# Kernel tuning notes

Hardware: AMD Instinct MI355X
Metric: run time of the kernel (lower is better)

The kernel has to match this reference:

```python
import jax, jax.numpy as jnp
import numpy as np

B, S, D, H, FF = 4, 2048, 1024, 16, 4096
HD = D // H
EPS = 1e-5


def layer_norm(x, g, b):
    mu = jnp.mean(x, axis=-1, keepdims=True)
    var = jnp.mean(jnp.square(x - mu), axis=-1, keepdims=True)
    return (x - mu) * jax.lax.rsqrt(var + EPS) * g + b


def setup_inputs() -> dict:
    key = jax.random.key(0)
    ks = jax.random.split(key, 8)
    s_d = 1.0 / np.sqrt(D)
    s_ff = 1.0 / np.sqrt(FF)
    return {
        "x": jax.random.normal(ks[0], (B, S, D), dtype=jnp.float32),
        "Wq": jax.random.normal(ks[1], (D, D), dtype=jnp.float32) * s_d,
        "bq": jnp.zeros((D,), jnp.float32),
        "Wk": jax.random.normal(ks[2], (D, D), dtype=jnp.float32) * s_d,
        "bk": jnp.zeros((D,), jnp.float32),
        "Wv": jax.random.normal(ks[3], (D, D), dtype=jnp.float32) * s_d,
        "bv": jnp.zeros((D,), jnp.float32),
        "g1": jnp.ones((D,), jnp.float32),
        "beta1": jnp.zeros((D,), jnp.float32),
        "g2": jnp.ones((D,), jnp.float32),
        "beta2": jnp.zeros((D,), jnp.float32),
        "W1": jax.random.normal(ks[4], (D, FF), dtype=jnp.float32) * s_d,
        "b1": jnp.zeros((FF,), jnp.float32),
        "W2": jax.random.normal(ks[5], (FF, D), dtype=jnp.float32) * s_ff,
        "b2": jnp.zeros((D,), jnp.float32),
    }


def reference(x, Wq, bq, Wk, bk, Wv, bv, g1, beta1, g2, beta2, W1, b1, W2, b2):
    # pre-LN attention (self.layer_norm in the original)
    h = layer_norm(x, g1, beta1)
    q = (h @ Wq + bq).reshape(B, S, H, HD)
    k = (h @ Wk + bk).reshape(B, S, H, HD)
    v = (h @ Wv + bv).reshape(B, S, H, HD)
    scores = jnp.einsum("bqhd,bkhd->bhqk", q, k) / np.sqrt(HD)
    probs = jax.nn.softmax(scores, axis=-1)
    attn = jnp.einsum("bhqk,bkhd->bqhd", probs, v).reshape(B, S, D)
    y = attn + x
    # second LN (self.LN), then FFN; note original adds residual from LN output
    f = layer_norm(y, g2, beta2)
    ff = jnp.maximum(f @ W1 + b1, 0.0) @ W2 + b2
    return f + ff
```

## Files before the change

### kernel.cpp

```cpp
#include <hip/hip_runtime.h>
#include <hip/hip_bf16.h>
#include <cstdint>
#include <cstddef>

#define B_   4
#define S_   2048
#define D_   1024
#define H_   16
#define HD_  64
#define FF_  4096
#define MTOT (B_*S_)

typedef __bf16 bf16;
typedef bf16  bf16x8 __attribute__((ext_vector_type(8)));
typedef bf16  bf16x4 __attribute__((ext_vector_type(4)));
typedef float f32x4  __attribute__((ext_vector_type(4)));

#define LOG2E 1.44269504088896340736f

__device__ __forceinline__ void async16(const bf16* g, bf16* l) {
  __builtin_amdgcn_global_load_lds(
      (const __attribute__((address_space(1))) unsigned int*)g,
      (__attribute__((address_space(3))) unsigned int*)l,
      16, 0, 0);
}

__global__ void wcast_t(const float* __restrict__ W, bf16* __restrict__ Wt,
                        int K, int N) {
  __shared__ float t[32][33];
  const int k0 = blockIdx.y * 32, n0 = blockIdx.x * 32;
  const int tx = threadIdx.x, ty = threadIdx.y;
#pragma unroll
  for (int r = ty; r < 32; r += 8)
    t[r][tx] = W[(size_t)(k0 + r) * N + n0 + tx];
  __syncthreads();
#pragma unroll
  for (int r = ty; r < 32; r += 8)
    Wt[(size_t)(n0 + r) * K + k0 + tx] = (bf16)t[tx][r];
}

__global__ void ln_fused(const float* __restrict__ xin, const float* __restrict__ res,
                         const float* __restrict__ gamma, const float* __restrict__ beta,
                         bf16* __restrict__ out) {
  const int row = blockIdx.x, tid = threadIdx.x;
  const int lane = tid & 63, w = tid >> 6;
  f32x4 v = *(const f32x4*)(xin + (size_t)row * D_ + tid * 4);
  if (res) {
    f32x4 r = *(const f32x4*)(res + (size_t)row * D_ + tid * 4);
    v += r;
  }
  float sum = v[0] + v[1] + v[2] + v[3];
  float sq  = v[0]*v[0] + v[1]*v[1] + v[2]*v[2] + v[3]*v[3];
#pragma unroll
  for (int d = 1; d < 64; d <<= 1) {
    sum += __shfl_xor(sum, d);
    sq  += __shfl_xor(sq, d);
  }
  __shared__ float red[8];
  if (lane == 0) { red[w] = sum; red[4 + w] = sq; }
  __syncthreads();
  sum = red[0] + red[1] + red[2] + red[3];
  sq  = red[4] + red[5] + red[6] + red[7];
  const float mu   = sum * (1.f / D_);
  const float rstd = rsqrtf(sq * (1.f / D_) - mu * mu + 1e-5f);
  f32x4 g  = *(const f32x4*)(gamma + tid * 4);
  f32x4 bt = *(const f32x4*)(beta  + tid * 4);
  bf16x4 ov;
#pragma unroll
  for (int j = 0; j < 4; j++)
    ov[j] = (bf16)((v[j] - mu) * rstd * g[j] + bt[j]);
  *(bf16x4*)(out + (size_t)row * D_ + tid * 4) = ov;
}

template <int EPI>
__global__ __launch_bounds__(512)
void gemm256(const bf16* __restrict__ A, const bf16* __restrict__ Bt,
             const float* __restrict__ bias, void* __restrict__ Cout,
             const bf16* __restrict__ addf,
             const float* __restrict__ bq, const float* __restrict__ bk,
             const float* __restrict__ bv, bf16* __restrict__ qout,
             bf16* __restrict__ kout, bf16* __restrict__ vtout,
             int M, int N, int K) {
  __shared__ bf16 As[2][256 * 64];
  __shared__ bf16 Bs[2][256 * 64];
  const int tid = threadIdx.x;
  const int lane = tid & 63;
  const int w = tid >> 6;
  const int wm = w >> 2, wn = w & 3;
  const int rg = lane >> 4, rl = lane & 15;
  const int sr = lane >> 3;
  const int sc = (lane & 7) ^ sr;

  const int nbn = N >> 8;
  const int cpx = (int)gridDim.x >> 3;
  const int bid = (int)blockIdx.x;
  const int swz = (bid & 7) * cpx + (bid >> 3);
  const int bm = (swz / nbn) << 8;
  const int bn = (swz % nbn) << 8;

  const bf16* gA0 = A  + (size_t)(bm + w * 8 + sr) * K + sc * 8;
  const bf16* gB0 = Bt + (size_t)(bn + w * 8 + sr) * K + sc * 8;
  const size_t i64K = (size_t)64 * K;

#define GSTAGE(slot, t)                                                        \
  {                                                                            \
    const bf16* ga_ = gA0 + (size_t)(t) * 64;                                  \
    const bf16* gb_ = gB0 + (size_t)(t) * 64;                                  \
    _Pragma("unroll")                                                          \
    for (int i_ = 0; i_ < 4; i_++) {                                           \
      async16(ga_ + i_ * i64K, &As[slot][(i_ * 64 + w * 8) * 64]);             \
      async16(gb_ + i_ * i64K, &Bs[slot][(i_ * 64 + w * 8) * 64]);             \
    }                                                                          \
  }

#define COMPUTE(slotbuf)                                                       \
  {                                                                            \
    const bf16* Ac = &As[slotbuf][0];                                          \
    const bf16* Bc = &Bs[slotbuf][0];                                          \
    _Pragma("unroll")                                                          \
    for (int kk = 0; kk < 2; kk++) {                                           \
      bf16x8 af[8], bw[4];                                                     \
      _Pragma("unroll")                                                        \
      for (int mi = 0; mi < 8; mi++)                                           \
        af[mi] = *(const bf16x8*)(Ac + (wm * 128 + mi * 16 + rl) * 64 +        \
                                  (((kk * 4 + rg) ^ (rl & 7)) * 8));           \
      _Pragma("unroll")                                                        \
      for (int ni = 0; ni < 4; ni++)                                           \
        bw[ni] = *(const bf16x8*)(Bc + (wn * 64 + ni * 16 + rl) * 64 +         \
                                  (((kk * 4 + rg) ^ (rl & 7)) * 8));           \
      _Pragma("unroll")                                                        \
      for (int mi = 0; mi < 8; mi++)                                           \
        _Pragma("unroll")                                                      \
        for (int ni = 0; ni < 4; ni++)                                         \
          acc[mi][ni] = __builtin_amdgcn_mfma_f32_16x16x32_bf16(               \
              af[mi], bw[ni], acc[mi][ni], 0, 0, 0);                           \
    }                                                                          \
  }

  f32x4 acc[8][4];
  const f32x4 z = {0.f, 0.f, 0.f, 0.f};
#pragma unroll
  for (int mi = 0; mi < 8; mi++)
#pragma unroll
    for (int ni = 0; ni < 4; ni++) acc[mi][ni] = z;

  const int NT = K >> 6;
  GSTAGE(0, 0);
  GSTAGE(1, 1);

  for (int t = 0; t < NT - 1; ++t) {
    asm volatile("s_waitcnt vmcnt(8)" ::: "memory");
    __builtin_amdgcn_sched_barrier(0);
    __builtin_amdgcn_s_barrier();
    __builtin_amdgcn_sched_barrier(0);
    COMPUTE(t & 1);
    __builtin_amdgcn_sched_barrier(0);
    __builtin_amdgcn_s_barrier();
    __builtin_amdgcn_sched_barrier(0);
    if (t + 2 < NT) GSTAGE(t & 1, t + 2);
  }
  asm volatile("s_waitcnt vmcnt(0)" ::: "memory");
  __builtin_amdgcn_sched_barrier(0);
  __builtin_amdgcn_s_barrier();
  __builtin_amdgcn_sched_barrier(0);
  COMPUTE((NT - 1) & 1);

#undef GSTAGE
#undef COMPUTE

#pragma unroll
  for (int mi = 0; mi < 8; mi++) {
    const int row0 = bm + wm * 128 + mi * 16 + rg * 4;
#pragma unroll
    for (int ni = 0; ni < 4; ni++) {
      const int col = bn + wn * 64 + ni * 16 + rl;
      if (EPI == 3) {
        const float bb = bias[col];
#pragma unroll
        for (int i = 0; i < 4; i++)
          ((bf16*)Cout)[(size_t)(row0 + i) * N + col] =
              (bf16)fmaxf(acc[mi][ni][i] + bb, 0.f);
      } else if (EPI == 4) {
        const float bb = bias[col];
#pragma unroll
        for (int i = 0; i < 4; i++)
          ((float*)Cout)[(size_t)(row0 + i) * N + col] =
              acc[mi][ni][i] + bb + (float)addf[(size_t)(row0 + i) * N + col];
      } else {
        const int sector = bn >> 10;
        const int cl = col & 1023;
        const float bb = (sector == 0) ? bq[cl] : (sector == 1 ? bk[cl] : bv[cl]);
#pragma unroll
        for (int i = 0; i < 4; i++) {
          const int row = row0 + i;
          const float v = acc[mi][ni][i] + bb;
          if (sector == 0) {
            qout[(size_t)row * D_ + cl] = (bf16)(v * (0.125f * LOG2E));
          } else if (sector == 1) {
            kout[(size_t)row * D_ + cl] = (bf16)v;
          } else {
            const int b = row >> 11, s = row & 2047;
            const int h = cl >> 6, hd = cl & 63;
            vtout[(((size_t)(b * H_ + h) * HD_ + hd) << 11) + s] = (bf16)v;
          }
        }
      }
    }
  }
}

__global__ __launch_bounds__(512, 4)
void attn_fwd(const bf16* __restrict__ Q, const bf16* __restrict__ Kb,
              const bf16* __restrict__ Vt, float* __restrict__ O) {
  __shared__ bf16 Ks[2][64 * 64];
  __shared__ bf16 Vs[2][64 * 64];
  __shared__ bf16 Pl[8][32][72];
  const int tid = threadIdx.x, lane = tid & 63, w = tid >> 6;
  const int rg = lane >> 4, rl = lane & 15;
  const int bh = blockIdx.y, b = bh >> 4, h = bh & 15;
  const int q0 = blockIdx.x * 256 + w * 32;

  const bf16* qp = Q + ((size_t)b * S_ + q0) * D_ + h * HD_;
  const bf16* kp = Kb + (size_t)b * S_ * D_ + h * HD_;
  const bf16* vp = Vt + (size_t)bh * HD_ * S_;

  const int sr = lane >> 3;
  const int sc = (lane & 7) ^ sr;

#define STAGE(buf, t)                                                          \
  {                                                                            \
    const int row = w * 8 + sr;                                                \
    async16(kp + (size_t)((t) * 64 + row) * D_ + sc * 8, &Ks[buf][w * 8 * 64]);\
    async16(vp + (size_t)row * S_ + (t) * 64 + sc * 8,  &Vs[buf][w * 8 * 64]); \
  }

  bf16x8 qf[2][2];
#pragma unroll
  for (int m = 0; m < 2; m++)
#pragma unroll
    for (int kc = 0; kc < 2; kc++)
      qf[m][kc] = *(const bf16x8*)(qp + (size_t)(m * 16 + rl) * D_ + kc * 32 + rg * 8);

  const f32x4 z = {0.f, 0.f, 0.f, 0.f};
  f32x4 o[2][4];
  float mr[2], lr[2];
#pragma unroll
  for (int m = 0; m < 2; m++) {
    mr[m] = -1e30f; lr[m] = 0.f;
#pragma unroll
    for (int np = 0; np < 4; np++) o[m][np] = z;
  }

  STAGE(0, 0);
  __syncthreads();

  int cur = 0;
  for (int t = 0; t < S_ / 64; ++t) {
    if (t + 1 < S_ / 64) STAGE(cur ^ 1, t + 1);
    const bf16* Kc = Ks[cur];
    const bf16* Vc = Vs[cur];

    bf16x8 kf[4][2];
#pragma unroll
    for (int n = 0; n < 4; n++) {
      const int krow = n * 16 + rl;
#pragma unroll
      for (int kc = 0; kc < 2; kc++)
        kf[n][kc] = *(const bf16x8*)(Kc + krow * 64 + (((kc * 4 + rg) ^ (krow & 7)) * 8));
    }

    f32x4 s[2][4];
#pragma unroll
    for (int m = 0; m < 2; m++)
#pragma unroll
      for (int n = 0; n < 4; n++) s[m][n] = z;
#pragma unroll
    for (int kc = 0; kc < 2; kc++)
#pragma unroll
      for (int n = 0; n < 4; n++)
#pragma unroll
        for (int m = 0; m < 2; m++)
          s[m][n] = __builtin_amdgcn_mfma_f32_16x16x32_bf16(kf[n][kc], qf[m][kc], s[m][n], 0, 0, 0);

#pragma unroll
    for (int m = 0; m < 2; m++) {
      float x0 = fmaxf(fmaxf(s[m][0][0], s[m][0][1]), fmaxf(s[m][0][2], s[m][0][3]));
      float x1 = fmaxf(fmaxf(s[m][1][0], s[m][1][1]), fmaxf(s[m][1][2], s[m][1][3]));
      float x2 = fmaxf(fmaxf(s[m][2][0], s[m][2][1]), fmaxf(s[m][2][2], s[m][2][3]));
      float x3 = fmaxf(fmaxf(s[m][3][0], s[m][3][1]), fmaxf(s[m][3][2], s[m][3][3]));
      float vmax = fmaxf(fmaxf(x0, x1), fmaxf(x2, x3));
      vmax = fmaxf(vmax, __shfl_xor(vmax, 16));
      vmax = fmaxf(vmax, __shfl_xor(vmax, 32));
      const float mnew = fmaxf(mr[m], vmax);
      const float corr = __builtin_amdgcn_exp2f(mr[m] - mnew);
      mr[m] = mnew;
      float ps = 0.f;
#pragma unroll
      for (int n = 0; n < 4; n++)
#pragma unroll
        for (int i = 0; i < 4; i++) {
          const float p = __builtin_amdgcn_exp2f(s[m][n][i] - mnew);
          s[m][n][i] = p;
          ps += p;
        }
      ps += __shfl_xor(ps, 16);
      ps += __shfl_xor(ps, 32);
      lr[m] = lr[m] * corr + ps;
#pragma unroll
      for (int np = 0; np < 4; np++)
#pragma unroll
        for (int i = 0; i < 4; i++) o[m][np][i] *= corr;
#pragma unroll
      for (int n = 0; n < 4; n++) {
        bf16x4 pv;
#pragma unroll
        for (int i = 0; i < 4; i++) pv[i] = (bf16)s[m][n][i];
        *(bf16x4*)&Pl[w][m * 16 + rl][n * 16 + rg * 4] = pv;
      }
    }

    bf16x8 pf[2][2];
#pragma unroll
    for (int m = 0; m < 2; m++)
#pragma unroll
      for (int kc = 0; kc < 2; kc++)
        pf[m][kc] = *(const bf16x8*)&Pl[w][m * 16 + rl][kc * 32 + rg * 8];

    bf16x8 vf[4][2];
#pragma unroll
    for (int np = 0; np < 4; np++) {
      const int vrow = np * 16 + rl;
#pragma unroll
      for (int kc = 0; kc < 2; kc++)
        vf[np][kc] = *(const bf16x8*)(Vc + vrow * 64 + (((kc * 4 + rg) ^ (vrow & 7)) * 8));
    }

#pragma unroll
    for (int kc = 0; kc < 2; kc++)
#pragma unroll
      for (int np = 0; np < 4; np++)
#pragma unroll
        for (int m = 0; m < 2; m++)
          o[m][np] = __builtin_amdgcn_mfma_f32_16x16x32_bf16(vf[np][kc], pf[m][kc], o[m][np], 0, 0, 0);

    __syncthreads();
    cur ^= 1;
  }
#undef STAGE

#pragma unroll
  for (int m = 0; m < 2; m++) {
    const float inv = 1.f / lr[m];
    const size_t rowb = ((size_t)b * S_ + q0 + m * 16 + rl) * D_ + h * HD_;
#pragma unroll
    for (int np = 0; np < 4; np++) {
      f32x4 ov;
#pragma unroll
      for (int i = 0; i < 4; i++) ov[i] = o[m][np][i] * inv;
      *(f32x4*)(O + rowb + np * 16 + rg * 4) = ov;
    }
  }
}

extern "C" void kernel_launch(void* const* d_in, const int* in_sizes, int n_in,
                              void* d_out, int out_size, void* d_ws, size_t ws_size,
                              hipStream_t stream) {
  (void)in_sizes; (void)n_in; (void)out_size; (void)ws_size;
  const float* x   = (const float*)d_in[0];
  const float* Wq  = (const float*)d_in[1];
  const float* bq  = (const float*)d_in[2];
  const float* Wk  = (const float*)d_in[3];
  const float* bk  = (const float*)d_in[4];
  const float* Wv  = (const float*)d_in[5];
  const float* bv  = (const float*)d_in[6];
  const float* g1  = (const float*)d_in[7];
  const float* be1 = (const float*)d_in[8];
  const float* g2  = (const float*)d_in[9];
  const float* be2 = (const float*)d_in[10];
  const float* W1  = (const float*)d_in[11];
  const float* b1  = (const float*)d_in[12];
  const float* W2  = (const float*)d_in[13];
  const float* b2  = (const float*)d_in[14];
  float* out = (float*)d_out;

  char* p = (char*)d_ws;
  const size_t MB = (size_t)1 << 20;
  bf16*  wqkv = (bf16*)(p + 0 * MB);
  bf16*  w1t  = (bf16*)(p + 6 * MB);
  bf16*  w2t  = (bf16*)(p + 14 * MB);
  bf16*  hb   = (bf16*)(p + 22 * MB);
  bf16*  qb   = (bf16*)(p + 38 * MB);
  bf16*  kb   = (bf16*)(p + 54 * MB);
  bf16*  vt   = (bf16*)(p + 70 * MB);
  float* at   = (float*)(p + 86 * MB);
  bf16*  fb   = (bf16*)(p + 118 * MB);
  bf16*  ff1  = (bf16*)(p + 22 * MB);

  const dim3 tb(32, 8);
  wcast_t<<<dim3(32, 32),  tb, 0, stream>>>(Wq, wqkv,                1024, 1024);
  wcast_t<<<dim3(32, 32),  tb, 0, stream>>>(Wk, wqkv + 1024 * 1024,  1024, 1024);
  wcast_t<<<dim3(32, 32),  tb, 0, stream>>>(Wv, wqkv + 2048 * 1024,  1024, 1024);
  wcast_t<<<dim3(128, 32), tb, 0, stream>>>(W1, w1t, 1024, 4096);
  wcast_t<<<dim3(32, 128), tb, 0, stream>>>(W2, w2t, 4096, 1024);

  ln_fused<<<MTOT, 256, 0, stream>>>(x, nullptr, g1, be1, hb);

  gemm256<5><<<384, 512, 0, stream>>>(hb, wqkv, nullptr, nullptr, nullptr,
                                      bq, bk, bv, qb, kb, vt, MTOT, 3072, 1024);

  attn_fwd<<<dim3(8, 64), 512, 0, stream>>>(qb, kb, vt, at);

  ln_fused<<<MTOT, 256, 0, stream>>>(at, x, g2, be2, fb);

  gemm256<3><<<512, 512, 0, stream>>>(fb, w1t, b1, ff1, nullptr,
                                      nullptr, nullptr, nullptr, nullptr, nullptr, nullptr,
                                      MTOT, 4096, 1024);
  gemm256<4><<<128, 512, 0, stream>>>(ff1, w2t, b2, out, fb,
                                      nullptr, nullptr, nullptr, nullptr, nullptr, nullptr,
                                      MTOT, 1024, 4096);
}
```

Measured before the change: 575.8 us.

## Rewrite GEMM as interleaved 8-phase pipeline and use 256x128 tiles for FFN2

Replaces the two-barrier double-buffered GEMM main loop with a finer-grained schedule. Each 64-wide K tile is split into two 32-wide halves, and the async loads for the next tile are issued between MFMA clusters with partial vmcnt waits and s_setprio raised around the MFMA clusters. The LDS layout is reorganised into K-half buffers with a new pair-row swizzle. The FFN2 GEMM switches to a 256x128 tile, which doubles its grid from 128 to 256 blocks so the device is better filled. The risks are a more fragile barrier and wait-count schedule and smaller per-wave reuse on the BN=128 path.

After: 531.1 us. -7.8%, faster.

```diff
diff --git a/kernel.cpp b/kernel.cpp
--- a/kernel.cpp
+++ b/kernel.cpp
@@ -23,6 +23,12 @@
       (const __attribute__((address_space(1))) unsigned int*)g,
       (__attribute__((address_space(3))) unsigned int*)l,
       16, 0, 0);
+}
+
+template <int N> __device__ __forceinline__ void vmw() {
+  if constexpr (N == 4)      asm volatile("s_waitcnt vmcnt(4)" ::: "memory");
+  else if constexpr (N == 3) asm volatile("s_waitcnt vmcnt(3)" ::: "memory");
+  else                       asm volatile("s_waitcnt vmcnt(0)" ::: "memory");
 }
 
 __global__ void wcast_t(const float* __restrict__ W, bf16* __restrict__ Wt,
@@ -72,105 +78,128 @@
   *(bf16x4*)(out + (size_t)row * D_ + tid * 4) = ov;
 }
 
-template <int EPI>
+template <int EPI, int BN>
 __global__ __launch_bounds__(512)
-void gemm256(const bf16* __restrict__ A, const bf16* __restrict__ Bt,
-             const float* __restrict__ bias, void* __restrict__ Cout,
-             const bf16* __restrict__ addf,
-             const float* __restrict__ bq, const float* __restrict__ bk,
-             const float* __restrict__ bv, bf16* __restrict__ qout,
-             bf16* __restrict__ kout, bf16* __restrict__ vtout,
-             int M, int N, int K) {
-  __shared__ bf16 As[2][256 * 64];
-  __shared__ bf16 Bs[2][256 * 64];
+void gemm8p(const bf16* __restrict__ Ag, const bf16* __restrict__ Bg,
+            const float* __restrict__ bias, void* __restrict__ Cout,
+            const bf16* __restrict__ addf,
+            const float* __restrict__ bq, const float* __restrict__ bk,
+            const float* __restrict__ bv, bf16* __restrict__ qout,
+            bf16* __restrict__ kout, bf16* __restrict__ vtout,
+            int M, int N, int K) {
+  constexpr int WN     = (BN == 256) ? 4 : 2;
+  constexpr int WMR    = (BN == 256) ? 128 : 64;
+  constexpr int AFR    = WMR / 16;
+  constexpr int BLOADS = BN / 128;
+  constexpr int BPHYS  = BN / 2;
+  constexpr int VMN    = 2 + BLOADS;
+
+  __shared__ bf16 As[2][2][128 * 64];
+  __shared__ bf16 Bs[2][2][BPHYS * 64];
+
   const int tid = threadIdx.x;
   const int lane = tid & 63;
   const int w = tid >> 6;
-  const int wm = w >> 2, wn = w & 3;
+  const int wm = w / WN, wn = w % WN;
   const int rg = lane >> 4, rl = lane & 15;
-  const int sr = lane >> 3;
-  const int sc = (lane & 7) ^ sr;
-
-  const int nbn = N >> 8;
+
+  const int sr    = lane >> 3;
+  const int scu   = (lane & 7) ^ sr;
+  const int srow  = w * 16 + 2 * sr + (scu >> 2);
+  const int sksub = (scu & 3) * 8;
+
+  const int nbn = N / BN;
   const int cpx = (int)gridDim.x >> 3;
   const int bid = (int)blockIdx.x;
   const int swz = (bid & 7) * cpx + (bid >> 3);
   const int bm = (swz / nbn) << 8;
-  const int bn = (swz % nbn) << 8;
-
-  const bf16* gA0 = A  + (size_t)(bm + w * 8 + sr) * K + sc * 8;
-  const bf16* gB0 = Bt + (size_t)(bn + w * 8 + sr) * K + sc * 8;
-  const size_t i64K = (size_t)64 * K;
-
-#define GSTAGE(slot, t)                                                        \
-  {                                                                            \
-    const bf16* ga_ = gA0 + (size_t)(t) * 64;                                  \
-    const bf16* gb_ = gB0 + (size_t)(t) * 64;                                  \
-    _Pragma("unroll")                                                          \
-    for (int i_ = 0; i_ < 4; i_++) {                                           \
-      async16(ga_ + i_ * i64K, &As[slot][(i_ * 64 + w * 8) * 64]);             \
-      async16(gb_ + i_ * i64K, &Bs[slot][(i_ * 64 + w * 8) * 64]);             \
-    }                                                                          \
-  }
-
-#define COMPUTE(slotbuf)                                                       \
-  {                                                                            \
-    const bf16* Ac = &As[slotbuf][0];                                          \
-    const bf16* Bc = &Bs[slotbuf][0];                                          \
-    _Pragma("unroll")                                                          \
-    for (int kk = 0; kk < 2; kk++) {                                           \
-      bf16x8 af[8], bw[4];                                                     \
-      _Pragma("unroll")                                                        \
-      for (int mi = 0; mi < 8; mi++)                                           \
-        af[mi] = *(const bf16x8*)(Ac + (wm * 128 + mi * 16 + rl) * 64 +        \
-                                  (((kk * 4 + rg) ^ (rl & 7)) * 8));           \
-      _Pragma("unroll")                                                        \
-      for (int ni = 0; ni < 4; ni++)                                           \
-        bw[ni] = *(const bf16x8*)(Bc + (wn * 64 + ni * 16 + rl) * 64 +         \
-                                  (((kk * 4 + rg) ^ (rl & 7)) * 8));           \
-      _Pragma("unroll")                                                        \
-      for (int mi = 0; mi < 8; mi++)                                           \
-        _Pragma("unroll")                                                      \
-        for (int ni = 0; ni < 4; ni++)                                         \
-          acc[mi][ni] = __builtin_amdgcn_mfma_f32_16x16x32_bf16(               \
-              af[mi], bw[ni], acc[mi][ni], 0, 0, 0);                           \
-    }                                                                          \
-  }
-
-  f32x4 acc[8][4];
+  const int bn = (swz % nbn) * BN;
+
+#define FRAG(arr, rr)                                                        \
+  ({ const int r_ = (rr); const int pr_ = r_ >> 1;                           \
+     const int c_ = ((((r_ & 1) << 2) | rg) ^ (pr_ & 7));                    \
+     *(const bf16x8*)(&(arr)[pr_ * 64 + c_ * 8]); })
+
+#define STAGE_A(oslot, kh, tt)                                               \
+  { _Pragma("unroll")                                                        \
+    for (int i_ = 0; i_ < 2; i_++)                                           \
+      async16(Ag + (size_t)(bm + i_ * 128 + srow) * K +                      \
+                  (size_t)((tt) * 64 + (kh) * 32 + sksub),                   \
+              &As[oslot][kh][(i_ * 64 + w * 8) * 64]); }
+
+#define STAGE_B(oslot, kh, tt)                                               \
+  { _Pragma("unroll")                                                        \
+    for (int i_ = 0; i_ < BLOADS; i_++)                                      \
+      async16(Bg + (size_t)(bn + i_ * 128 + srow) * K +                      \
+                  (size_t)((tt) * 64 + (kh) * 32 + sksub),                   \
+              &Bs[oslot][kh][(i_ * 64 + w * 8) * 64]); }
+
+#define BAR()                                                                \
+  { __builtin_amdgcn_sched_barrier(0); __builtin_amdgcn_s_barrier();         \
+    __builtin_amdgcn_sched_barrier(0); }
+
+#define MMACL(nh, B0, B1)                                                    \
+  { __builtin_amdgcn_s_setprio(1);                                           \
+    _Pragma("unroll")                                                        \
+    for (int mi = 0; mi < AFR; mi++) {                                       \
+      acc[mi][(nh)*2+0] = __builtin_amdgcn_mfma_f32_16x16x32_bf16(           \
+          af[mi], B0, acc[mi][(nh)*2+0], 0, 0, 0);                           \
+      acc[mi][(nh)*2+1] = __builtin_amdgcn_mfma_f32_16x16x32_bf16(           \
+          af[mi], B1, acc[mi][(nh)*2+1], 0, 0, 0);                           \
+    }                                                                        \
+    __builtin_amdgcn_s_setprio(0); }
+
+#define TILE(slot, oslot, tnx)                                               \
+  { bf16x8 af[AFR];                                                          \
+    _Pragma("unroll")                                                        \
+    for (int mi = 0; mi < AFR; mi++)                                         \
+      af[mi] = FRAG(As[slot][0], wm * WMR + mi * 16 + rl);                   \
+    { bf16x8 b0 = FRAG(Bs[slot][0], wn * 64 + 0  + rl);                      \
+      bf16x8 b1 = FRAG(Bs[slot][0], wn * 64 + 16 + rl);                      \
+      STAGE_A(oslot, 0, tnx); BAR(); MMACL(0, b0, b1); }                     \
+    { bf16x8 b0 = FRAG(Bs[slot][0], wn * 64 + 32 + rl);                      \
+      bf16x8 b1 = FRAG(Bs[slot][0], wn * 64 + 48 + rl);                      \
+      STAGE_B(oslot, 0, tnx); vmw<VMN>(); BAR(); MMACL(1, b0, b1); }         \
+    _Pragma("unroll")                                                        \
+    for (int mi = 0; mi < AFR; mi++)                                         \
+      af[mi] = FRAG(As[slot][1], wm * WMR + mi * 16 + rl);                   \
+    { bf16x8 b0 = FRAG(Bs[slot][1], wn * 64 + 0  + rl);                      \
+      bf16x8 b1 = FRAG(Bs[slot][1], wn * 64 + 16 + rl);                      \
+      STAGE_A(oslot, 1, tnx); BAR(); MMACL(0, b0, b1); }                     \
+    { bf16x8 b0 = FRAG(Bs[slot][1], wn * 64 + 32 + rl);                      \
+      bf16x8 b1 = FRAG(Bs[slot][1], wn * 64 + 48 + rl);                      \
+      STAGE_B(oslot, 1, tnx); vmw<VMN>(); BAR(); MMACL(1, b0, b1); } }
+
+  f32x4 acc[AFR][4];
   const f32x4 z = {0.f, 0.f, 0.f, 0.f};
 #pragma unroll
-  for (int mi = 0; mi < 8; mi++)
+  for (int mi = 0; mi < AFR; mi++)
 #pragma unroll
     for (int ni = 0; ni < 4; ni++) acc[mi][ni] = z;
 
   const int NT = K >> 6;
-  GSTAGE(0, 0);
-  GSTAGE(1, 1);
-
-  for (int t = 0; t < NT - 1; ++t) {
-    asm volatile("s_waitcnt vmcnt(8)" ::: "memory");
-    __builtin_amdgcn_sched_barrier(0);
-    __builtin_amdgcn_s_barrier();
-    __builtin_amdgcn_sched_barrier(0);
-    COMPUTE(t & 1);
-    __builtin_amdgcn_sched_barrier(0);
-    __builtin_amdgcn_s_barrier();
-    __builtin_amdgcn_sched_barrier(0);
-    if (t + 2 < NT) GSTAGE(t & 1, t + 2);
-  }
-  asm volatile("s_waitcnt vmcnt(0)" ::: "memory");
-  __builtin_amdgcn_sched_barrier(0);
-  __builtin_amdgcn_s_barrier();
-  __builtin_amdgcn_sched_barrier(0);
-  COMPUTE((NT - 1) & 1);
-
-#undef GSTAGE
-#undef COMPUTE
-
-#pragma unroll
-  for (int mi = 0; mi < 8; mi++) {
-    const int row0 = bm + wm * 128 + mi * 16 + rg * 4;
+  STAGE_A(0, 0, 0); STAGE_B(0, 0, 0); STAGE_A(0, 1, 0); STAGE_B(0, 1, 0);
+  vmw<VMN>();
+  BAR();
+
+  for (int it = 0; it < NT / 2; ++it) {
+    const int t1 = 2 * it + 1;
+    const int n2 = (t1 + 1 < NT) ? t1 + 1 : NT - 1;
+    TILE(0, 1, t1);
+    TILE(1, 0, n2);
+  }
+  vmw<0>();
+
+#undef TILE
+#undef MMACL
+#undef BAR
+#undef STAGE_B
+#undef STAGE_A
+#undef FRAG
+
+#pragma unroll
+  for (int mi = 0; mi < AFR; mi++) {
+    const int row0 = bm + wm * WMR + mi * 16 + rg * 4;
 #pragma unroll
     for (int ni = 0; ni < 4; ni++) {
       const int col = bn + wn * 64 + ni * 16 + rl;
@@ -405,17 +434,17 @@
 
   ln_fused<<<MTOT, 256, 0, stream>>>(x, nullptr, g1, be1, hb);
 
-  gemm256<5><<<384, 512, 0, stream>>>(hb, wqkv, nullptr, nullptr, nullptr,
-                                      bq, bk, bv, qb, kb, vt, MTOT, 3072, 1024);
+  gemm8p<5, 256><<<384, 512, 0, stream>>>(hb, wqkv, nullptr, nullptr, nullptr,
+                                          bq, bk, bv, qb, kb, vt, MTOT, 3072, 1024);
 
   attn_fwd<<<dim3(8, 64), 512, 0, stream>>>(qb, kb, vt, at);
 
   ln_fused<<<MTOT, 256, 0, stream>>>(at, x, g2, be2, fb);
 
-  gemm256<3><<<512, 512, 0, stream>>>(fb, w1t, b1, ff1, nullptr,
-                                      nullptr, nullptr, nullptr, nullptr, nullptr, nullptr,
-                                      MTOT, 4096, 1024);
-  gemm256<4><<<128, 512, 0, stream>>>(ff1, w2t, b2, out, fb,
-                                      nullptr, nullptr, nullptr, nullptr, nullptr, nullptr,
-                                      MTOT, 1024, 4096);
-}
+  gemm8p<3, 256><<<512, 512, 0, stream>>>(fb, w1t, b1, ff1, nullptr,
+                                          nullptr, nullptr, nullptr, nullptr, nullptr, nullptr,
+                                          MTOT, 4096, 1024);
+  gemm8p<4, 128><<<256, 512, 0, stream>>>(ff1, w2t, b2, out, fb,
+                                          nullptr, nullptr, nullptr, nullptr, nullptr, nullptr,
+                                          MTOT, 1024, 4096);
+}
```
